# Kernel optimization log

Measured on AMD Instinct MI355X. Metric: run time of the kernel, lower is better.

## Reference

```python
import jax, jax.numpy as jnp
import numpy as np

B, DX, DZ, DY = 8192, 512, 1024, 256


def setup_inputs() -> dict:
    key = jax.random.key(0)
    ks = jax.random.split(key, 13)
    s = 0.02
    return {
        "xs": jax.random.normal(ks[0], (B, DX), dtype=jnp.float32),
        "Wx": jax.random.normal(ks[1], (DZ, DX), dtype=jnp.float32) * s,
        "bx": jnp.zeros((DZ,), dtype=jnp.float32),
        "Wy": jax.random.normal(ks[2], (DZ, DY), dtype=jnp.float32) * s,
        "by": jnp.zeros((DZ,), dtype=jnp.float32),
        "Wn": jax.random.normal(ks[3], (DZ, 3 * DZ), dtype=jnp.float32) * s,
        "bn": jnp.zeros((DZ,), dtype=jnp.float32),
        "Wu": jax.random.normal(ks[4], (DY, DZ), dtype=jnp.float32) * s,
        "bu": jnp.zeros((DY,), dtype=jnp.float32),
        "Wq": jax.random.normal(ks[5], (DY, DZ), dtype=jnp.float32) * s,
        "bq": jnp.zeros((DY,), dtype=jnp.float32),
        "ys_init": jax.random.normal(ks[6], (B, DY), dtype=jnp.float32),
        "zs_init": jax.random.normal(ks[7], (B, DZ), dtype=jnp.float32),
        "T": 4,
        "n": 6,
    }


def reference(xs, Wx, bx, Wy, by, Wn, bn, Wu, bu, Wq, bq, ys_init, zs_init, T, n):
    xs_e = xs @ Wx.T + bx                      # [B, DZ]
    ys_e = ys_init @ Wy.T + by                 # [B, DZ]
    zs = zs_init                               # [B, DZ]
    null = jnp.zeros_like(xs_e)

    def query(x, y, z):
        w = jnp.concatenate([x, y, z], axis=-1)  # [B, 3*DZ]
        return jnp.tanh(w @ Wn.T + bn)

    # no-grad refinement (T-1 outer iterations)
    for _ in range(T - 1):
        for _ in range(n):
            zs = query(xs_e, ys_e, zs)
        ys_e = query(null, ys_e, zs)
    ys_e = jax.lax.stop_gradient(ys_e)
    zs = jax.lax.stop_gradient(zs)

    # final grad-enabled block
    for _ in range(n):
        zs = query(xs_e, ys_e, zs)
    ys_e = query(null, ys_e, zs)

    y_hat = jax.nn.sigmoid(ys_e @ Wu.T + bu)
    q_hat = jax.nn.sigmoid(ys_e @ Wq.T + bq)
    return (y_hat, q_hat)
```

## Files before the change

kernel.cpp:

```cpp
#include <hip/hip_runtime.h>
#include <hip/hip_bf16.h>
#include <cstdint>
#include <cstddef>

#define B_   8192
#define DX_  512
#define DZ_  1024
#define DY_  256
#define T_   4
#define NN_  6

typedef float f32x4 __attribute__((ext_vector_type(4)));
typedef short s16x8 __attribute__((ext_vector_type(8)));
typedef long i64x2 __attribute__((ext_vector_type(2)));
typedef __hip_bfloat16 bf16;

__device__ __forceinline__ void gload_lds16(const void* g, void* l) {
  __builtin_amdgcn_global_load_lds(
      (const __attribute__((address_space(1))) void*)g,
      (__attribute__((address_space(3))) void*)l,
      16, 0, 0);
}

__device__ __forceinline__ float bf2f(unsigned short u) {
  union { unsigned int i; float f; } cv; cv.i = ((unsigned int)u) << 16; return cv.f;
}

__device__ __forceinline__ int permb(int n) {
  return (n & ~63) | (((n >> 3) & 3) << 4) | (((n >> 5) & 1) << 3) | (n & 7);
}

__device__ __forceinline__ void cv4(const float* __restrict__ s, bf16* __restrict__ d, long i) {
  float4 v = ((const float4*)s)[i];
  ushort4 o;
  bf16 a0 = __float2bfloat16(v.x); o.x = *(unsigned short*)&a0;
  bf16 a1 = __float2bfloat16(v.y); o.y = *(unsigned short*)&a1;
  bf16 a2 = __float2bfloat16(v.z); o.z = *(unsigned short*)&a2;
  bf16 a3 = __float2bfloat16(v.w); o.w = *(unsigned short*)&a3;
  ((ushort4*)d)[i] = o;
}
__device__ __forceinline__ void cv4f8(const float* __restrict__ src, unsigned char* __restrict__ dst,
                                      long row, int k0, int srcld, int srcoff) {
  float4 v = *(const float4*)(src + row * srcld + srcoff + k0);
  int p = __builtin_amdgcn_cvt_pk_fp8_f32(v.x, v.y, 0, 0);
  p = __builtin_amdgcn_cvt_pk_fp8_f32(v.z, v.w, p, 1);
  *(int*)(dst + row * DZ_ + permb(k0)) = p;
}

__global__ void cvt_all_kernel(const float* __restrict__ Wn, const float* __restrict__ Wx,
                               const float* __restrict__ Wy, const float* __restrict__ Wu,
                               const float* __restrict__ Wq, const float* __restrict__ xs,
                               const float* __restrict__ ys0, const float* __restrict__ zs0,
                               const float* __restrict__ bu, const float* __restrict__ bq,
                               bf16* __restrict__ Wn_b, bf16* __restrict__ Wx_b,
                               bf16* __restrict__ Wy_b, bf16* __restrict__ Wuq_b,
                               bf16* __restrict__ xs_b, bf16* __restrict__ ysin_b,
                               bf16* __restrict__ z_a, float* __restrict__ buq,
                               unsigned char* __restrict__ Wnz8, unsigned char* __restrict__ z_a8) {
  const long NWN = (long)DZ_ * 3 * DZ_ / 4, NWX = (long)DZ_ * DX_ / 4,
             NWY = (long)DZ_ * DY_ / 4,     NWU = (long)DY_ * DZ_ / 4,
             NXS = (long)B_ * DX_ / 4,      NYS = (long)B_ * DY_ / 4,
             NZS = (long)B_ * DZ_ / 4,      NBQ = 2 * DY_ / 4,
             NW8 = (long)DZ_ * DZ_ / 4,     NZ8 = (long)B_ * DZ_ / 4;
  const long total = NWN + NWX + NWY + 2 * NWU + NXS + NYS + NZS + NBQ + NW8 + NZ8;
  for (long i = (long)blockIdx.x * blockDim.x + threadIdx.x; i < total;
       i += (long)gridDim.x * blockDim.x) {
    long j = i;
    if (j < NWN) { cv4(Wn, Wn_b, j); continue; } j -= NWN;
    if (j < NWX) { cv4(Wx, Wx_b, j); continue; } j -= NWX;
    if (j < NWY) { cv4(Wy, Wy_b, j); continue; } j -= NWY;
    if (j < NWU) { cv4(Wu, Wuq_b, j); continue; } j -= NWU;
    if (j < NWU) { cv4(Wq, Wuq_b + (size_t)DY_ * DZ_, j); continue; } j -= NWU;
    if (j < NXS) { cv4(xs, xs_b, j); continue; } j -= NXS;
    if (j < NYS) { cv4(ys0, ysin_b, j); continue; } j -= NYS;
    if (j < NZS) { cv4(zs0, z_a, j); continue; } j -= NZS;
    if (j < NBQ) {
      float4 v = (j < DY_ / 4) ? ((const float4*)bu)[j] : ((const float4*)bq)[j - DY_ / 4];
      ((float4*)buq)[j] = v; continue;
    } j -= NBQ;
    if (j < NW8) {
      long e = j * 4; long row = e >> 10; int k0 = (int)(e & 1023);
      cv4f8(Wn, Wnz8, row, k0, 3 * DZ_, 2 * DZ_); continue;
    } j -= NW8;
    {
      long e = j * 4; long row = e >> 10; int k0 = (int)(e & 1023);
      cv4f8(zs0, z_a8, row, k0, DZ_, 0);
    }
  }
}

template<int ACT, int MODE, bool HASADD>
__global__ __launch_bounds__(512, 2)
void gemm_bt(const bf16* __restrict__ A, int lda,
             const bf16* __restrict__ W, int ldw,
             const float* __restrict__ bias,
             const bf16* __restrict__ add1,
             bf16* __restrict__ out_pre,
             void* __restrict__ out, void* __restrict__ out2,
             int N, int K)
{
  __shared__ __align__(16) char ldsc[3 * 49152];
  const int t    = threadIdx.x;
  const int lane = t & 63;
  const int wave = t >> 6;
  const int m0 = blockIdx.x * 256;
  const int n0 = blockIdx.y * 128;

  const int srow = t >> 3;
  const int q    = (t & 7) ^ ((t >> 3) & 7);
  const bf16* gA = A + (size_t)(m0 + srow) * lda + q * 8;
  const bf16* gB = W + (size_t)(n0 + srow) * ldw + q * 8;
  const int wb = wave * 1024;

  auto stage = [&](int kt) {
    char* base = ldsc + (kt % 3) * 49152;
    const int ko = kt << 6;
#pragma unroll
    for (int i = 0; i < 4; ++i)
      gload_lds16(gA + (size_t)(i * 64) * lda + ko, base + i * 8192 + wb);
#pragma unroll
    for (int i = 0; i < 2; ++i)
      gload_lds16(gB + (size_t)(i * 64) * ldw + ko, base + 32768 + i * 8192 + wb);
  };

  const int mo = (wave >> 1) * 64;
  const int no = (wave & 1) * 64;
  const int fr = lane & 15;
  const int g4 = lane >> 4;
  const int rb = g4 * 4;

  const int NT = K >> 6;

  float bv[4] = {0.f, 0.f, 0.f, 0.f};
  if (bias) {
#pragma unroll
    for (int j = 0; j < 4; ++j) bv[j] = bias[n0 + no + j * 16 + fr];
  }
  unsigned short adr[4][4][4];
  if (HASADD && MODE != 1) {
#pragma unroll
    for (int f = 0; f < 4; ++f)
#pragma unroll
      for (int j = 0; j < 4; ++j) {
        const unsigned short* p = (const unsigned short*)add1
            + (size_t)(m0 + mo + f * 16 + rb) * N + (n0 + no + j * 16 + fr);
#pragma unroll
        for (int r = 0; r < 4; ++r) adr[f][j][r] = p[(size_t)r * N];
      }
  }
  __builtin_amdgcn_sched_barrier(0);
  stage(0);
  stage(1);
  __builtin_amdgcn_sched_barrier(0);

  f32x4 acc[4][4];
#pragma unroll
  for (int f = 0; f < 4; ++f)
#pragma unroll
    for (int j = 0; j < 4; ++j)
#pragma unroll
      for (int r = 0; r < 4; ++r) {
        float v = bv[j];
        if (HASADD && MODE != 1) v += bf2f(adr[f][j][r]);
        acc[f][j][r] = v;
      }

  s16x8 a0[4], b0[4], a1[4], b1[4];
  auto ldfrags = [&](int kt, int s, s16x8* fa, s16x8* fb) {
    const char* pA = ldsc + (kt % 3) * 49152;
    const char* pB = pA + 32768;
    const int cb = ((s * 4 + g4) ^ (fr & 7)) * 16;
#pragma unroll
    for (int f = 0; f < 4; ++f) fa[f] = *(const s16x8*)(pA + (mo + f * 16 + fr) * 128 + cb);
#pragma unroll
    for (int j = 0; j < 4; ++j) fb[j] = *(const s16x8*)(pB + (no + j * 16 + fr) * 128 + cb);
  };
  auto domfma = [&](const s16x8* fa, const s16x8* fb) {
    __builtin_amdgcn_s_setprio(1);
#pragma unroll
    for (int f = 0; f < 4; ++f)
#pragma unroll
      for (int j = 0; j < 4; ++j)
        acc[f][j] = __builtin_amdgcn_mfma_f32_16x16x32_bf16(fa[f], fb[j], acc[f][j], 0, 0, 0);
    __builtin_amdgcn_s_setprio(0);
  };

  asm volatile("s_waitcnt vmcnt(6)" ::: "memory");
  __builtin_amdgcn_s_barrier();
  __builtin_amdgcn_sched_barrier(0);

  for (int kt = 0; kt < NT; ++kt) {
    ldfrags(kt, 0, a0, b0);
    ldfrags(kt, 1, a1, b1);
    if (kt + 2 < NT) stage(kt + 2);
    __builtin_amdgcn_sched_barrier(0);
    asm volatile("s_waitcnt lgkmcnt(8)" ::: "memory");
    __builtin_amdgcn_sched_barrier(0);
    domfma(a0, b0);
    asm volatile("s_waitcnt lgkmcnt(0)" ::: "memory");
    __builtin_amdgcn_sched_barrier(0);
    domfma(a1, b1);
    if (kt + 2 < NT)      asm volatile("s_waitcnt vmcnt(6)" ::: "memory");
    else if (kt + 1 < NT) asm volatile("s_waitcnt vmcnt(0)" ::: "memory");
    if (kt + 1 < NT) {
      __builtin_amdgcn_s_barrier();
      __builtin_amdgcn_sched_barrier(0);
    }
  }

#pragma unroll
  for (int f = 0; f < 4; ++f) {
#pragma unroll
    for (int j = 0; j < 4; ++j) {
      const int n = n0 + no + j * 16 + fr;
#pragma unroll
      for (int r = 0; r < 4; ++r) {
        const int m = m0 + mo + f * 16 + rb + r;
        float v = acc[f][j][r];
        if (MODE == 1) {
          out_pre[(size_t)m * N + n] = __float2bfloat16(v);
          v += bf2f(((const unsigned short*)add1)[(size_t)m * N + n]);
        }
        if (ACT == 1)      { float e = __expf(2.f * v); v = 1.f - 2.f / (e + 1.f); }
        else if (ACT == 2) v = 1.f / (1.f + __expf(-v));
        if (MODE == 2) {
          if (n < DY_) ((float*)out)[(size_t)m * DY_ + n] = v;
          else         ((float*)out2)[(size_t)m * DY_ + (n - DY_)] = v;
        } else {
          ((bf16*)out)[(size_t)m * N + n] = __float2bfloat16(v);
        }
      }
    }
  }
}

__global__ __launch_bounds__(512, 2)
void gemm_f8(const unsigned char* __restrict__ A8,
             const unsigned char* __restrict__ W8,
             const bf16* __restrict__ add1,
             unsigned char* __restrict__ out8,
             bf16* __restrict__ out16)
{
  __shared__ __align__(16) char ldsc[4 * 24576];
  const int t    = threadIdx.x;
  const int lane = t & 63;
  const int wave = t >> 6;
  const int m0 = blockIdx.x * 256;
  const int n0 = blockIdx.y * 128;

  const int srow = t >> 2;
  const int q    = (t & 3) ^ ((t >> 3) & 3);
  const unsigned char* gA = A8 + (size_t)(m0 + srow) * DZ_ + q * 16;
  const unsigned char* gB = W8 + (size_t)(n0 + srow) * DZ_ + q * 16;
  const int wb = wave * 1024;

  auto stage = [&](int kt) {
    char* base = ldsc + (kt & 3) * 24576;
    const int ko = kt << 6;
    gload_lds16(gA + ko, base + wb);
    gload_lds16(gA + (size_t)128 * DZ_ + ko, base + 8192 + wb);
    gload_lds16(gB + ko, base + 16384 + wb);
  };

  const int mo = (wave >> 1) * 64;
  const int no = (wave & 1) * 64;
  const int fr = lane & 15;
  const int g4 = lane >> 4;
  const int rb = g4 * 4;
  const int cb = (g4 ^ ((fr >> 1) & 3)) * 16;

  const int NT = DZ_ >> 6;

  unsigned short adr[4][4][4];
#pragma unroll
  for (int f = 0; f < 4; ++f)
#pragma unroll
    for (int j = 0; j < 4; ++j) {
      const unsigned short* p = (const unsigned short*)add1
          + (size_t)(m0 + mo + f * 16 + rb) * DZ_ + (n0 + no + j * 16 + fr);
#pragma unroll
      for (int r = 0; r < 4; ++r) adr[f][j][r] = p[(size_t)r * DZ_];
    }
  __builtin_amdgcn_sched_barrier(0);
  stage(0); stage(1); stage(2);
  __builtin_amdgcn_sched_barrier(0);

  f32x4 acc[4][4];
#pragma unroll
  for (int f = 0; f < 4; ++f)
#pragma unroll
    for (int j = 0; j < 4; ++j)
#pragma unroll
      for (int r = 0; r < 4; ++r) acc[f][j][r] = bf2f(adr[f][j][r]);

  asm volatile("s_waitcnt vmcnt(6)" ::: "memory");
  __builtin_amdgcn_s_barrier();
  __builtin_amdgcn_sched_barrier(0);

  for (int kt = 0; kt < NT; ++kt) {
    const char* pA = ldsc + (kt & 3) * 24576;
    const char* pB = pA + 16384;
    i64x2 av[4], bv[4];
#pragma unroll
    for (int f = 0; f < 4; ++f) av[f] = *(const i64x2*)(pA + (mo + f * 16 + fr) * 64 + cb);
#pragma unroll
    for (int j = 0; j < 4; ++j) bv[j] = *(const i64x2*)(pB + (no + j * 16 + fr) * 64 + cb);
    if (kt + 3 < NT) stage(kt + 3);
    __builtin_amdgcn_sched_barrier(0);
    asm volatile("s_waitcnt lgkmcnt(0)" ::: "memory");
    __builtin_amdgcn_sched_barrier(0);
    __builtin_amdgcn_s_setprio(1);
#pragma unroll
    for (int f = 0; f < 4; ++f)
#pragma unroll
      for (int j = 0; j < 4; ++j) {
        acc[f][j] = __builtin_amdgcn_mfma_f32_16x16x32_fp8_fp8(av[f][0], bv[j][0], acc[f][j], 0, 0, 0);
        acc[f][j] = __builtin_amdgcn_mfma_f32_16x16x32_fp8_fp8(av[f][1], bv[j][1], acc[f][j], 0, 0, 0);
      }
    __builtin_amdgcn_s_setprio(0);
    const int rem = NT - 1 - kt;
    if (rem >= 3)      asm volatile("s_waitcnt vmcnt(6)" ::: "memory");
    else if (rem == 2) asm volatile("s_waitcnt vmcnt(3)" ::: "memory");
    else if (rem == 1) asm volatile("s_waitcnt vmcnt(0)" ::: "memory");
    if (rem >= 1) {
      __builtin_amdgcn_s_barrier();
      __builtin_amdgcn_sched_barrier(0);
    }
  }

#pragma unroll
  for (int f = 0; f < 4; ++f) {
#pragma unroll
    for (int j = 0; j < 4; ++j) {
      const int n = n0 + no + j * 16 + fr;
      const int np = permb(n);
#pragma unroll
      for (int r = 0; r < 4; ++r) {
        const int m = m0 + mo + f * 16 + rb + r;
        float v = acc[f][j][r];
        float e = __expf(2.f * v); v = 1.f - 2.f / (e + 1.f);
        out8[(size_t)m * DZ_ + np] =
            (unsigned char)__builtin_amdgcn_cvt_pk_fp8_f32(v, v, 0, 0);
        if (out16) out16[(size_t)m * DZ_ + n] = __float2bfloat16(v);
      }
    }
  }
}

extern "C" void kernel_launch(void* const* d_in, const int* in_sizes, int n_in,
                              void* d_out, int out_size, void* d_ws, size_t ws_size,
                              hipStream_t stream) {
  const float* xs  = (const float*)d_in[0];
  const float* Wx  = (const float*)d_in[1];
  const float* bx  = (const float*)d_in[2];
  const float* Wy  = (const float*)d_in[3];
  const float* by  = (const float*)d_in[4];
  const float* Wn  = (const float*)d_in[5];
  const float* bn  = (const float*)d_in[6];
  const float* Wu  = (const float*)d_in[7];
  const float* bu  = (const float*)d_in[8];
  const float* Wq  = (const float*)d_in[9];
  const float* bq  = (const float*)d_in[10];
  const float* ys0 = (const float*)d_in[11];
  const float* zs0 = (const float*)d_in[12];

  char* ws = (char*)d_ws;
  size_t off = 0;
  auto take = [&](size_t bytes) -> char* {
    char* p = ws + off;
    off += (bytes + 255) & ~(size_t)255;
    return p;
  };

  bf16*  Wn_b   = (bf16*)take((size_t)DZ_ * 3 * DZ_ * 2);
  bf16*  Wx_b   = (bf16*)take((size_t)DZ_ * DX_ * 2);
  bf16*  Wy_b   = (bf16*)take((size_t)DZ_ * DY_ * 2);
  bf16*  Wuq_b  = (bf16*)take((size_t)2 * DY_ * DZ_ * 2);
  float* buq    = (float*)take((size_t)2 * DY_ * 4);
  bf16*  ys_b   = (bf16*)take((size_t)B_ * DZ_ * 2);
  bf16*  z_a    = (bf16*)take((size_t)B_ * DZ_ * 2);
  bf16*  z_b    = (bf16*)take((size_t)B_ * DZ_ * 2);
  bf16*  cx     = (bf16*)take((size_t)B_ * DZ_ * 2);
  bf16*  cy     = (bf16*)take((size_t)B_ * DZ_ * 2);
  bf16*  c      = (bf16*)take((size_t)B_ * DZ_ * 2);
  unsigned char* Wnz8 = (unsigned char*)take((size_t)DZ_ * DZ_);
  unsigned char* z_a8 = (unsigned char*)take((size_t)B_ * DZ_);
  unsigned char* z_b8 = (unsigned char*)take((size_t)B_ * DZ_);
  bf16* xs_b   = c;
  bf16* ysin_b = (bf16*)((char*)c + (size_t)B_ * DX_ * 2);
  bf16* xse_b  = cy;

  cvt_all_kernel<<<2048, 256, 0, stream>>>(Wn, Wx, Wy, Wu, Wq, xs, ys0, zs0, bu, bq,
                                           Wn_b, Wx_b, Wy_b, Wuq_b,
                                           xs_b, ysin_b, z_a, buq, Wnz8, z_a8);

  const dim3 blk(512);
  const dim3 gz(B_ / 256, DZ_ / 128);
  const dim3 gh(B_ / 256, 4);

  gemm_bt<0, 0, false><<<gz, blk, 0, stream>>>(xs_b, DX_, Wx_b, DX_, bx, nullptr, nullptr, xse_b, nullptr, DZ_, DX_);
  gemm_bt<0, 0, false><<<gz, blk, 0, stream>>>(ysin_b, DY_, Wy_b, DY_, by, nullptr, nullptr, ys_b, nullptr, DZ_, DY_);
  gemm_bt<0, 0, false><<<gz, blk, 0, stream>>>(xse_b, DZ_, Wn_b, 3 * DZ_, nullptr, nullptr, nullptr, cx, nullptr, DZ_, DZ_);

  bf16* zc = z_a;
  bf16* zn = z_b;
  unsigned char* zc8 = z_a8;
  unsigned char* zn8 = z_b8;
  for (int tt = 0; tt < T_; ++tt) {
    gemm_bt<0, 1, true><<<gz, blk, 0, stream>>>(ys_b, DZ_, Wn_b + DZ_, 3 * DZ_, bn, cx, cy, c, nullptr, DZ_, DZ_);
    if (tt < T_ - 1) {
      for (int i = 0; i < NN_; ++i) {
        gemm_f8<<<gz, blk, 0, stream>>>(zc8, Wnz8, c, zn8, (i == NN_ - 1) ? zn : nullptr);
        unsigned char* t8 = zc8; zc8 = zn8; zn8 = t8;
      }
      bf16* tmp = zc; zc = zn; zn = tmp;
    } else {
      for (int i = 0; i < NN_; ++i) {
        gemm_bt<1, 0, true><<<gz, blk, 0, stream>>>(zc, DZ_, Wn_b + 2 * DZ_, 3 * DZ_, nullptr, c, nullptr, zn, nullptr, DZ_, DZ_);
        bf16* tmp = zc; zc = zn; zn = tmp;
      }
    }
    gemm_bt<1, 0, true><<<gz, blk, 0, stream>>>(zc, DZ_, Wn_b + 2 * DZ_, 3 * DZ_, nullptr, cy, nullptr, ys_b, nullptr, DZ_, DZ_);
  }

  float* outp = (float*)d_out;
  gemm_bt<2, 2, false><<<gh, blk, 0, stream>>>(ys_b, DZ_, Wuq_b, DZ_, buq, nullptr, nullptr,
                                               outp, outp + (size_t)B_ * DY_, 2 * DY_, DZ_);
}
```

Baseline: 828.9 us.

## Use FP8 for refinement y-queries, drop zs bf16 conversion, retile bf16 GEMM K

The bf16 GEMM now stages K in 32-wide slices with a 4-deep LDS ring and a matching swizzle, replacing the 64-wide 3-deep ring. The ys update in the no-grad refinement iterations now runs through the FP8 GEMM instead of the bf16 one. Only the last no-grad z step writes a bf16 shadow copy, so zs_init no longer needs converting to bf16. This cuts bf16 GEMM work and conversion traffic, at the cost of lower precision for the ys updates and a different pipelining depth with more loop iterations.

```diff
diff --git a/kernel.cpp b/kernel.cpp
--- a/kernel.cpp
+++ b/kernel.cpp
@@ -55,14 +55,14 @@
                                bf16* __restrict__ Wn_b, bf16* __restrict__ Wx_b,
                                bf16* __restrict__ Wy_b, bf16* __restrict__ Wuq_b,
                                bf16* __restrict__ xs_b, bf16* __restrict__ ysin_b,
-                               bf16* __restrict__ z_a, float* __restrict__ buq,
+                               float* __restrict__ buq,
                                unsigned char* __restrict__ Wnz8, unsigned char* __restrict__ z_a8) {
   const long NWN = (long)DZ_ * 3 * DZ_ / 4, NWX = (long)DZ_ * DX_ / 4,
              NWY = (long)DZ_ * DY_ / 4,     NWU = (long)DY_ * DZ_ / 4,
              NXS = (long)B_ * DX_ / 4,      NYS = (long)B_ * DY_ / 4,
-             NZS = (long)B_ * DZ_ / 4,      NBQ = 2 * DY_ / 4,
+             NBQ = 2 * DY_ / 4,
              NW8 = (long)DZ_ * DZ_ / 4,     NZ8 = (long)B_ * DZ_ / 4;
-  const long total = NWN + NWX + NWY + 2 * NWU + NXS + NYS + NZS + NBQ + NW8 + NZ8;
+  const long total = NWN + NWX + NWY + 2 * NWU + NXS + NYS + NBQ + NW8 + NZ8;
   for (long i = (long)blockIdx.x * blockDim.x + threadIdx.x; i < total;
        i += (long)gridDim.x * blockDim.x) {
     long j = i;
@@ -73,7 +73,6 @@
     if (j < NWU) { cv4(Wq, Wuq_b + (size_t)DY_ * DZ_, j); continue; } j -= NWU;
     if (j < NXS) { cv4(xs, xs_b, j); continue; } j -= NXS;
     if (j < NYS) { cv4(ys0, ysin_b, j); continue; } j -= NYS;
-    if (j < NZS) { cv4(zs0, z_a, j); continue; } j -= NZS;
     if (j < NBQ) {
       float4 v = (j < DY_ / 4) ? ((const float4*)bu)[j] : ((const float4*)bq)[j - DY_ / 4];
       ((float4*)buq)[j] = v; continue;
@@ -99,28 +98,25 @@
              void* __restrict__ out, void* __restrict__ out2,
              int N, int K)
 {
-  __shared__ __align__(16) char ldsc[3 * 49152];
+  __shared__ __align__(16) char ldsc[4 * 24576];
   const int t    = threadIdx.x;
   const int lane = t & 63;
   const int wave = t >> 6;
   const int m0 = blockIdx.x * 256;
   const int n0 = blockIdx.y * 128;
 
-  const int srow = t >> 3;
-  const int q    = (t & 7) ^ ((t >> 3) & 7);
+  const int srow = t >> 2;
+  const int q    = (t & 3) ^ ((t >> 3) & 3);
   const bf16* gA = A + (size_t)(m0 + srow) * lda + q * 8;
   const bf16* gB = W + (size_t)(n0 + srow) * ldw + q * 8;
   const int wb = wave * 1024;
 
   auto stage = [&](int kt) {
-    char* base = ldsc + (kt % 3) * 49152;
-    const int ko = kt << 6;
-#pragma unroll
-    for (int i = 0; i < 4; ++i)
-      gload_lds16(gA + (size_t)(i * 64) * lda + ko, base + i * 8192 + wb);
-#pragma unroll
-    for (int i = 0; i < 2; ++i)
-      gload_lds16(gB + (size_t)(i * 64) * ldw + ko, base + 32768 + i * 8192 + wb);
+    char* base = ldsc + (kt & 3) * 24576;
+    const int ko = kt << 5;
+    gload_lds16(gA + ko, base + wb);
+    gload_lds16(gA + (size_t)128 * lda + ko, base + 8192 + wb);
+    gload_lds16(gB + ko, base + 16384 + wb);
   };
 
   const int mo = (wave >> 1) * 64;
@@ -128,8 +124,9 @@
   const int fr = lane & 15;
   const int g4 = lane >> 4;
   const int rb = g4 * 4;
-
-  const int NT = K >> 6;
+  const int cb = (g4 ^ ((fr >> 1) & 3)) * 16;
+
+  const int NT = K >> 5;
 
   float bv[4] = {0.f, 0.f, 0.f, 0.f};
   if (bias) {
@@ -149,8 +146,7 @@
       }
   }
   __builtin_amdgcn_sched_barrier(0);
-  stage(0);
-  stage(1);
+  stage(0); stage(1); stage(2);
   __builtin_amdgcn_sched_barrier(0);
 
   f32x4 acc[4][4];
@@ -165,17 +161,22 @@
         acc[f][j][r] = v;
       }
 
-  s16x8 a0[4], b0[4], a1[4], b1[4];
-  auto ldfrags = [&](int kt, int s, s16x8* fa, s16x8* fb) {
-    const char* pA = ldsc + (kt % 3) * 49152;
-    const char* pB = pA + 32768;
-    const int cb = ((s * 4 + g4) ^ (fr & 7)) * 16;
-#pragma unroll
-    for (int f = 0; f < 4; ++f) fa[f] = *(const s16x8*)(pA + (mo + f * 16 + fr) * 128 + cb);
-#pragma unroll
-    for (int j = 0; j < 4; ++j) fb[j] = *(const s16x8*)(pB + (no + j * 16 + fr) * 128 + cb);
-  };
-  auto domfma = [&](const s16x8* fa, const s16x8* fb) {
+  asm volatile("s_waitcnt vmcnt(6)" ::: "memory");
+  __builtin_amdgcn_s_barrier();
+  __builtin_amdgcn_sched_barrier(0);
+
+  for (int kt = 0; kt < NT; ++kt) {
+    const char* pA = ldsc + (kt & 3) * 24576;
+    const char* pB = pA + 16384;
+    s16x8 fa[4], fb[4];
+#pragma unroll
+    for (int f = 0; f < 4; ++f) fa[f] = *(const s16x8*)(pA + (mo + f * 16 + fr) * 64 + cb);
+#pragma unroll
+    for (int j = 0; j < 4; ++j) fb[j] = *(const s16x8*)(pB + (no + j * 16 + fr) * 64 + cb);
+    if (kt + 3 < NT) stage(kt + 3);
+    __builtin_amdgcn_sched_barrier(0);
+    asm volatile("s_waitcnt lgkmcnt(0)" ::: "memory");
+    __builtin_amdgcn_sched_barrier(0);
     __builtin_amdgcn_s_setprio(1);
 #pragma unroll
     for (int f = 0; f < 4; ++f)
@@ -183,26 +184,11 @@
       for (int j = 0; j < 4; ++j)
         acc[f][j] = __builtin_amdgcn_mfma_f32_16x16x32_bf16(fa[f], fb[j], acc[f][j], 0, 0, 0);
     __builtin_amdgcn_s_setprio(0);
-  };
-
-  asm volatile("s_waitcnt vmcnt(6)" ::: "memory");
-  __builtin_amdgcn_s_barrier();
-  __builtin_amdgcn_sched_barrier(0);
-
-  for (int kt = 0; kt < NT; ++kt) {
-    ldfrags(kt, 0, a0, b0);
-    ldfrags(kt, 1, a1, b1);
-    if (kt + 2 < NT) stage(kt + 2);
-    __builtin_amdgcn_sched_barrier(0);
-    asm volatile("s_waitcnt lgkmcnt(8)" ::: "memory");
-    __builtin_amdgcn_sched_barrier(0);
-    domfma(a0, b0);
-    asm volatile("s_waitcnt lgkmcnt(0)" ::: "memory");
-    __builtin_amdgcn_sched_barrier(0);
-    domfma(a1, b1);
-    if (kt + 2 < NT)      asm volatile("s_waitcnt vmcnt(6)" ::: "memory");
-    else if (kt + 1 < NT) asm volatile("s_waitcnt vmcnt(0)" ::: "memory");
-    if (kt + 1 < NT) {
+    const int rem = NT - 1 - kt;
+    if (rem >= 3)      asm volatile("s_waitcnt vmcnt(6)" ::: "memory");
+    else if (rem == 2) asm volatile("s_waitcnt vmcnt(3)" ::: "memory");
+    else if (rem == 1) asm volatile("s_waitcnt vmcnt(0)" ::: "memory");
+    if (rem >= 1) {
       __builtin_amdgcn_s_barrier();
       __builtin_amdgcn_sched_barrier(0);
     }
@@ -339,7 +325,7 @@
         const int m = m0 + mo + f * 16 + rb + r;
         float v = acc[f][j][r];
         float e = __expf(2.f * v); v = 1.f - 2.f / (e + 1.f);
-        out8[(size_t)m * DZ_ + np] =
+        if (out8)  out8[(size_t)m * DZ_ + np] =
             (unsigned char)__builtin_amdgcn_cvt_pk_fp8_f32(v, v, 0, 0);
         if (out16) out16[(size_t)m * DZ_ + n] = __float2bfloat16(v);
       }
@@ -392,7 +378,7 @@
 
   cvt_all_kernel<<<2048, 256, 0, stream>>>(Wn, Wx, Wy, Wu, Wq, xs, ys0, zs0, bu, bq,
                                            Wn_b, Wx_b, Wy_b, Wuq_b,
-                                           xs_b, ysin_b, z_a, buq, Wnz8, z_a8);
+                                           xs_b, ysin_b, buq, Wnz8, z_a8);
 
   const dim3 blk(512);
   const dim3 gz(B_ / 256, DZ_ / 128);
@@ -402,25 +388,26 @@
   gemm_bt<0, 0, false><<<gz, blk, 0, stream>>>(ysin_b, DY_, Wy_b, DY_, by, nullptr, nullptr, ys_b, nullptr, DZ_, DY_);
   gemm_bt<0, 0, false><<<gz, blk, 0, stream>>>(xse_b, DZ_, Wn_b, 3 * DZ_, nullptr, nullptr, nullptr, cx, nullptr, DZ_, DZ_);
 
-  bf16* zc = z_a;
-  bf16* zn = z_b;
   unsigned char* zc8 = z_a8;
   unsigned char* zn8 = z_b8;
   for (int tt = 0; tt < T_; ++tt) {
     gemm_bt<0, 1, true><<<gz, blk, 0, stream>>>(ys_b, DZ_, Wn_b + DZ_, 3 * DZ_, bn, cx, cy, c, nullptr, DZ_, DZ_);
     if (tt < T_ - 1) {
       for (int i = 0; i < NN_; ++i) {
-        gemm_f8<<<gz, blk, 0, stream>>>(zc8, Wnz8, c, zn8, (i == NN_ - 1) ? zn : nullptr);
+        bf16* shadow = (tt == T_ - 2 && i == NN_ - 1) ? z_a : nullptr;
+        gemm_f8<<<gz, blk, 0, stream>>>(zc8, Wnz8, c, zn8, shadow);
         unsigned char* t8 = zc8; zc8 = zn8; zn8 = t8;
       }
-      bf16* tmp = zc; zc = zn; zn = tmp;
+      gemm_f8<<<gz, blk, 0, stream>>>(zc8, Wnz8, cy, nullptr, ys_b);
     } else {
+      bf16* zc = z_a;
+      bf16* zn = z_b;
       for (int i = 0; i < NN_; ++i) {
         gemm_bt<1, 0, true><<<gz, blk, 0, stream>>>(zc, DZ_, Wn_b + 2 * DZ_, 3 * DZ_, nullptr, c, nullptr, zn, nullptr, DZ_, DZ_);
         bf16* tmp = zc; zc = zn; zn = tmp;
       }
-    }
-    gemm_bt<1, 0, true><<<gz, blk, 0, stream>>>(zc, DZ_, Wn_b + 2 * DZ_, 3 * DZ_, nullptr, cy, nullptr, ys_b, nullptr, DZ_, DZ_);
+      gemm_bt<1, 0, true><<<gz, blk, 0, stream>>>(zc, DZ_, Wn_b + 2 * DZ_, 3 * DZ_, nullptr, cy, nullptr, ys_b, nullptr, DZ_, DZ_);
+    }
   }
 
   float* outp = (float*)d_out;
```

After: 829.8 us. Within noise of the previous version (+0.1%).
